# Kernel optimization log

Measured on AMD Instinct MI355X. Metric: run time of the kernel, lower is better.

## Reference

```python
import jax, jax.numpy as jnp
import numpy as np

D_MODEL = 1024
D_STATE = 16
D_CONV = 4
EXPAND = 2
HEADDIM = 64
NGROUPS = 1
D_INNER = EXPAND * D_MODEL            # 2048
NHEADS = D_INNER // HEADDIM           # 32
CONV_DIM = D_INNER + 2 * NGROUPS * D_STATE   # 2080
D_IN_PROJ = 2 * D_INNER + 2 * NGROUPS * D_STATE + NHEADS  # 4160
EPS = 1e-5
BATCH, SEQLEN = 4, 2048


def setup_inputs() -> dict:
    key = jax.random.key(0)
    ks = jax.random.split(key, 8)
    x = jax.random.normal(ks[0], (BATCH, SEQLEN, D_MODEL), jnp.float32)
    W_in = jax.random.normal(ks[1], (D_MODEL, D_IN_PROJ), jnp.float32) * 0.02
    conv_w = jax.random.normal(ks[2], (CONV_DIM, D_CONV), jnp.float32) * 0.2
    conv_b = jnp.zeros((CONV_DIM,), jnp.float32)
    # dt_bias = inverse softplus of dt drawn in [1e-3, 1e-1] (mamba_ssm init)
    dt = jax.random.uniform(ks[3], (NHEADS,), jnp.float32, 0.001, 0.1)
    dt_bias = jnp.log(jnp.expm1(dt))
    A_log = jnp.log(jax.random.uniform(ks[4], (NHEADS,), jnp.float32, 1.0, 16.0))
    D_param = jnp.ones((NHEADS,), jnp.float32)
    norm_w = jnp.ones((D_INNER,), jnp.float32)
    W_out = jax.random.normal(ks[5], (D_INNER, D_MODEL), jnp.float32) * 0.02
    layer_scale = jnp.full((D_MODEL,), 1e-4, jnp.float32)
    return dict(x=x, W_in=W_in, conv_w=conv_w, conv_b=conv_b, dt_bias=dt_bias,
                A_log=A_log, D_param=D_param, norm_w=norm_w, W_out=W_out,
                layer_scale=layer_scale)


def _silu(v):
    return v * jax.nn.sigmoid(v)


def _mamba2(x, W_in, conv_w, conv_b, dt_bias, A_log, D_param, norm_w, W_out):
    b, l, _ = x.shape
    zxbcdt = x @ W_in                                  # (b, l, d_in_proj)
    z = zxbcdt[..., :D_INNER]                          # gate
    xBC = zxbcdt[..., D_INNER:D_INNER + CONV_DIM]
    dt = jax.nn.softplus(zxbcdt[..., D_INNER + CONV_DIM:] + dt_bias)  # (b, l, h)
    # causal depthwise conv1d (kernel D_CONV) + SiLU
    xp = jnp.pad(xBC, ((0, 0), (D_CONV - 1, 0), (0, 0)))
    conv = sum(xp[:, k:k + l, :] * conv_w[:, k] for k in range(D_CONV)) + conv_b
    xBC = _silu(conv)
    xs = xBC[..., :D_INNER].reshape(b, l, NHEADS, HEADDIM)  # (b, l, h, p)
    Bm = xBC[..., D_INNER:D_INNER + D_STATE]                # (b, l, n), ngroups=1
    Cm = xBC[..., D_INNER + D_STATE:]                       # (b, l, n)
    A = -jnp.exp(A_log)                                     # (h,)
    dA = jnp.exp(dt * A)                                    # (b, l, h)
    dtx = dt[..., None] * xs                                # (b, l, h, p)

    def step(h, inp):
        dA_t, dtx_t, B_t, C_t = inp
        # h: (b, h, p, n)
        h = h * dA_t[..., None, None] + dtx_t[..., None] * B_t[:, None, None, :]
        y = jnp.einsum('bhpn,bn->bhp', h, C_t)
        return h, y

    h0 = jnp.zeros((b, NHEADS, HEADDIM, D_STATE), x.dtype)
    _, ys = jax.lax.scan(step, h0, (dA.transpose(1, 0, 2), dtx.transpose(1, 0, 2, 3),
                                    Bm.transpose(1, 0, 2), Cm.transpose(1, 0, 2)))
    y = ys.transpose(1, 0, 2, 3) + D_param[None, None, :, None] * xs  # (b, l, h, p)
    y = y.reshape(b, l, D_INNER)
    # gated RMSNorm (norm_before_gate=False): gate first, then rmsnorm
    y = y * _silu(z)
    y = y * jax.lax.rsqrt(jnp.mean(y * y, axis=-1, keepdims=True) + EPS) * norm_w
    return y @ W_out


def reference(x, W_in, conv_w, conv_b, dt_bias, A_log, D_param, norm_w, W_out, layer_scale):
    # dropout is identity (eval / p=0)
    return x + _mamba2(x, W_in, conv_w, conv_b, dt_bias, A_log, D_param, norm_w, W_out) * layer_scale
```

## Files before the change

### kernel.cpp

```cpp
#include <hip/hip_runtime.h>
#include <hip/hip_bf16.h>

#define D_MODEL   1024
#define D_STATE   16
#define D_CONV    4
#define HEADDIM   64
#define NHEADS    32
#define D_INNER   2048
#define CONV_DIM  2080
#define D_IN_PROJ 4160
#define NPAD      4224
#define BATCH     4
#define SEQLEN    2048
#define MROWS     (BATCH*SEQLEN)
#define QCHUNK    64
#define NCHUNK    (SEQLEN/QCHUNK)
#define DT_COL    (2*D_INNER + 2*D_STATE)

#define WSCALE    16.f
#define YSCALE    64.f

__device__ __forceinline__ unsigned short f2b(float f) {
    union { float f; unsigned int u; } v; v.f = f;
    unsigned int r = (v.u + 0x7FFFu + ((v.u >> 16) & 1u)) >> 16;
    return (unsigned short)r;
}
__device__ __forceinline__ float b2f(unsigned short h) {
    union { unsigned int u; float f; } v; v.u = ((unsigned int)h) << 16;
    return v.f;
}
__device__ __forceinline__ unsigned char f2fp8(float f) {
    return (unsigned char)(__builtin_amdgcn_cvt_pk_fp8_f32(f, 0.f, 0, false) & 0xFF);
}

typedef __attribute__((ext_vector_type(8))) short bf16x8;
typedef __attribute__((ext_vector_type(4))) float f32x4;
typedef __attribute__((ext_vector_type(4))) int   i32x4;
typedef __attribute__((ext_vector_type(8))) int   i32x8;

__device__ __forceinline__ i32x8 cat8(i32x4 a, i32x4 b) {
    i32x8 r;
    r[0] = a[0]; r[1] = a[1]; r[2] = a[2]; r[3] = a[3];
    r[4] = b[0]; r[5] = b[1]; r[6] = b[2]; r[7] = b[3];
    return r;
}

__device__ __forceinline__ void async_copy16b(const unsigned char* g, unsigned char* l) {
    __builtin_amdgcn_global_load_lds(
        (const __attribute__((address_space(1))) void*)g,
        (__attribute__((address_space(3))) void*)l, 16, 0, 0);
}

__global__ void cast_f32_fp8(const float* __restrict__ in, unsigned char* __restrict__ out, int n) {
    int i = (blockIdx.x * blockDim.x + threadIdx.x) * 4;
    if (i >= n) return;
    float4 v = *(const float4*)&in[i];
    int p = __builtin_amdgcn_cvt_pk_fp8_f32(v.x, v.y, 0, false);
    p = __builtin_amdgcn_cvt_pk_fp8_f32(v.z, v.w, p, true);
    *(unsigned int*)&out[i] = (unsigned int)p;
}

__global__ void transpose_both(const float* __restrict__ W_in, unsigned char* __restrict__ winT,
                               const float* __restrict__ W_out, unsigned char* __restrict__ woutT,
                               const float* __restrict__ norm_w) {
    __shared__ float tile[64][65];
    int bid = blockIdx.x;
    const float* W; unsigned char* WT; const float* kscale;
    int K, N, bx, by;
    if (bid < 1056) { W = W_in;  WT = winT;  kscale = nullptr; K = 1024; N = 4160; bx = bid % 66; by = bid / 66; }
    else { bid -= 1056; W = W_out; WT = woutT; kscale = norm_w; K = 2048; N = 1024; bx = bid % 16; by = bid / 16; }
    int n0 = bx * 64, k0 = by * 64;
    int tx = threadIdx.x & 63, ty = threadIdx.x >> 6;
    #pragma unroll
    for (int i = 0; i < 16; i++) {
        int r = ty * 16 + i;
        int n = n0 + tx;
        float v = (n < N) ? W[(size_t)(k0 + r) * N + n] : 0.f;
        tile[r][tx] = v;
    }
    __syncthreads();
    float ks = WSCALE * (kscale ? kscale[k0 + tx] : 1.f);
    #pragma unroll
    for (int i = 0; i < 16; i++) {
        int r = ty * 16 + i;
        WT[(size_t)(n0 + r) * K + k0 + tx] = f2fp8(tile[tx][r] * ks);
    }
}

template <int EPI>
__global__ __launch_bounds__(256)
void gemm_fp8(const unsigned char* __restrict__ A, const unsigned char* __restrict__ B,
              int K, int N, unsigned short* __restrict__ Cb,
              float* __restrict__ Cf, const float* __restrict__ xres,
              const float* __restrict__ ls, const float* __restrict__ rs) {
    __shared__ unsigned char lds_a[128 * 128];
    __shared__ unsigned char lds_b[128 * 128];
    const int tid  = threadIdx.x;
    const int wave = tid >> 6;
    const int lane = tid & 63;
    const int bid = blockIdx.x;
    const int xcd = bid & 7, g = bid >> 3;
    const int bm = xcd * 8 + (g & 7);
    const int bn = g >> 3;
    const int wm = wave >> 1, wn = wave & 1;

    f32x4 acc[4][4];
    #pragma unroll
    for (int i = 0; i < 4; i++)
        #pragma unroll
        for (int j = 0; j < 4; j++) acc[i][j] = (f32x4){0.f, 0.f, 0.f, 0.f};

    const int srow = lane >> 3;
    const int sseg = (lane & 7) ^ srow;
    const unsigned char* gA0 = A + (size_t)(bm * 128 + wave * 8 + srow) * K + sseg * 16;
    const unsigned char* gB0 = B + (size_t)(bn * 128 + wave * 8 + srow) * K + sseg * 16;
    const int ldsbase = wave * 8 * 128;

    const int lm = lane & 15, q = lane >> 4;

    for (int k0 = 0; k0 < K; k0 += 128) {
        #pragma unroll
        for (int j = 0; j < 4; j++) {
            async_copy16b(gA0 + k0 + (size_t)(j * 32) * K, &lds_a[ldsbase + j * 32 * 128]);
            async_copy16b(gB0 + k0 + (size_t)(j * 32) * K, &lds_b[ldsbase + j * 32 * 128]);
        }
        __syncthreads();

        i32x8 af[4], bfr[4];
        #pragma unroll
        for (int i = 0; i < 4; i++) {
            int r = wm * 64 + i * 16 + lm;
            int s0 = ((2 * q) ^ (r & 7)) * 16, s1 = ((2 * q + 1) ^ (r & 7)) * 16;
            af[i] = cat8(*(const i32x4*)&lds_a[r * 128 + s0],
                         *(const i32x4*)&lds_a[r * 128 + s1]);
        }
        #pragma unroll
        for (int j = 0; j < 4; j++) {
            int r = wn * 64 + j * 16 + lm;
            int s0 = ((2 * q) ^ (r & 7)) * 16, s1 = ((2 * q + 1) ^ (r & 7)) * 16;
            bfr[j] = cat8(*(const i32x4*)&lds_b[r * 128 + s0],
                          *(const i32x4*)&lds_b[r * 128 + s1]);
        }
        #pragma unroll
        for (int i = 0; i < 4; i++)
            #pragma unroll
            for (int j = 0; j < 4; j++)
                acc[i][j] = __builtin_amdgcn_mfma_scale_f32_16x16x128_f8f6f4(
                    af[i], bfr[j], acc[i][j], 0, 0,
                    0, 0x7F7F7F7F, 0, 0x7F7F7F7F);
        __syncthreads();
    }

    const int row0 = bm * 128 + wm * 64;
    const int col0 = bn * 128 + wn * 64;
    const int lq = (lane >> 4) * 4;
    #pragma unroll
    for (int i = 0; i < 4; i++) {
        #pragma unroll
        for (int j = 0; j < 4; j++) {
            #pragma unroll
            for (int r = 0; r < 4; r++) {
                int gr = row0 + i * 16 + lq + r;
                int gc = col0 + j * 16 + lm;
                float v = acc[i][j][r];
                if (EPI == 0) {
                    Cb[(size_t)gr * N + gc] = f2b(v * (1.f / WSCALE));
                } else {
                    size_t idx = (size_t)gr * 1024 + gc;
                    Cf[idx] = xres[idx] + v * ls[gc] * rs[gr] * (1.f / (WSCALE * YSCALE));
                }
            }
        }
    }
}

__global__ __launch_bounds__(256)
void ssd_hcomp(const unsigned short* __restrict__ zx, const float* __restrict__ dt_bias,
               const float* __restrict__ conv_w, const float* __restrict__ conv_b,
               const float* __restrict__ A_log,
               float* __restrict__ hbuf, float* __restrict__ pbuf,
               unsigned short* __restrict__ xTg, unsigned short* __restrict__ bcg,
               float* __restrict__ scA) {
    __shared__ unsigned short sXraw[67 * 64];
    __shared__ unsigned short sBCraw[67 * 32];
    __shared__ unsigned short sXT[64 * 72];
    __shared__ unsigned short sBC[64 * 32];
    __shared__ unsigned short sBwT[16 * 72];
    __shared__ float sdt[64], scd[64];

    const int blk = blockIdx.x;
    const int c  = blk & 31;
    const int h  = (blk >> 5) & 31;
    const int b  = blk >> 10;
    const int bh = blk >> 5;
    const int row0 = b * SEQLEN + c * QCHUNK;
    const int batch0 = b * SEQLEN;

    const int t    = threadIdx.x;
    const int w    = t >> 6;
    const int lane = t & 63;
    const int lm   = lane & 15;
    const int lq8  = (lane >> 4) * 8;
    const int lq4  = (lane >> 4) * 4;
    const float Ah = -__expf(A_log[h]);

    for (int i = t; i < 536; i += 256) {
        int r = i >> 3, seg = i & 7;
        int gr = row0 - 3 + r;
        int4 v = (gr >= batch0) ? *(const int4*)&zx[(size_t)gr * NPAD + D_INNER + h * 64 + seg * 8]
                                : (int4){0, 0, 0, 0};
        *(int4*)&sXraw[r * 64 + seg * 8] = v;
    }
    for (int i = t; i < 268; i += 256) {
        int r = i >> 2, seg = i & 3;
        int gr = row0 - 3 + r;
        int4 v = (gr >= batch0) ? *(const int4*)&zx[(size_t)gr * NPAD + 2 * D_INNER + seg * 8]
                                : (int4){0, 0, 0, 0};
        *(int4*)&sBCraw[r * 32 + seg * 8] = v;
    }
    if (t < 64) {
        float raw = b2f(zx[(size_t)(row0 + t) * NPAD + DT_COL + h]) + dt_bias[h];
        float dtv = (raw > 20.f) ? raw : log1pf(__expf(raw));
        float v = dtv;
        #pragma unroll
        for (int o = 1; o < 64; o <<= 1) {
            float u = __shfl_up(v, o, 64);
            if (t >= o) v += u;
        }
        sdt[t] = dtv;
        scd[t] = v;
        float sc = __expf(Ah * v);
        float* scrow = &scA[(size_t)(bh * NCHUNK + c) * 192];
        scrow[t] = dtv; scrow[64 + t] = v; scrow[128 + t] = sc;
        if (t == 63) pbuf[bh * NCHUNK + c] = sc;
    }
    __syncthreads();

    {
        const int p = t & 63, sblk = (t >> 6) * 16;
        const int ch = h * 64 + p;
        const float4 cw = *(const float4*)&conv_w[ch * 4];
        const float cb = conv_b[ch];
        float x0 = b2f(sXraw[(sblk + 0) * 64 + p]);
        float x1 = b2f(sXraw[(sblk + 1) * 64 + p]);
        float x2 = b2f(sXraw[(sblk + 2) * 64 + p]);
        #pragma unroll
        for (int i = 0; i < 16; i++) {
            float x3 = b2f(sXraw[(sblk + i + 3) * 64 + p]);
            float acc = cb + cw.x * x0 + cw.y * x1 + cw.z * x2 + cw.w * x3;
            float sv = acc / (1.f + __expf(-acc));
            sXT[p * 72 + sblk + i] = f2b(sv);
            x0 = x1; x1 = x2; x2 = x3;
        }
    }
    {
        const int ch32 = t & 31, s0 = (t >> 5) * 8;
        const int ch = D_INNER + ch32;
        const float4 cw = *(const float4*)&conv_w[ch * 4];
        const float cb = conv_b[ch];
        const float cdl = scd[63];
        float x0 = b2f(sBCraw[(s0 + 0) * 32 + ch32]);
        float x1 = b2f(sBCraw[(s0 + 1) * 32 + ch32]);
        float x2 = b2f(sBCraw[(s0 + 2) * 32 + ch32]);
        #pragma unroll
        for (int i = 0; i < 8; i++) {
            int s = s0 + i;
            float x3 = b2f(sBCraw[(s + 3) * 32 + ch32]);
            float acc = cb + cw.x * x0 + cw.y * x1 + cw.z * x2 + cw.w * x3;
            float sv = acc / (1.f + __expf(-acc));
            sBC[s * 32 + ch32] = f2b(sv);
            if (ch32 < 16) {
                float wgt = sdt[s] * __expf(Ah * (cdl - scd[s]));
                sBwT[ch32 * 72 + s] = f2b(sv * wgt);
            }
            x0 = x1; x1 = x2; x2 = x3;
        }
    }
    __syncthreads();

    f32x4 hacc = (f32x4){0.f, 0.f, 0.f, 0.f};
    #pragma unroll
    for (int ks = 0; ks < 2; ks++) {
        bf16x8 af = *(const bf16x8*)&sBwT[lm * 72 + ks * 32 + lq8];
        bf16x8 bf_ = *(const bf16x8*)&sXT[(w * 16 + lm) * 72 + ks * 32 + lq8];
        hacc = __builtin_amdgcn_mfma_f32_16x16x32_bf16(af, bf_, hacc, 0, 0, 0);
    }
    #pragma unroll
    for (int r = 0; r < 4; r++)
        hbuf[(size_t)(bh * NCHUNK + c) * 1024 + (lq4 + r) * 64 + (w * 16 + lm)] = hacc[r];

    #pragma unroll
    for (int it = 0; it < 2; it++) {
        int idx = t + it * 256;
        int p = idx >> 3, seg = idx & 7;
        *(int4*)&xTg[(size_t)(bh * 64 + p) * SEQLEN + c * 64 + seg * 8] =
            *(const int4*)&sXT[p * 72 + seg * 8];
    }
    if (h == 0) {
        int s = t >> 2, seg = t & 3;
        *(int4*)&bcg[(size_t)(b * SEQLEN + c * 64 + s) * 32 + seg * 8] =
            *(const int4*)&sBC[s * 32 + seg * 8];
    }
}

__global__ __launch_bounds__(1024)
void ssd_state_scan(float* __restrict__ hbuf, const float* __restrict__ pbuf) {
    int bh = blockIdx.x;
    int t = threadIdx.x;
    __shared__ float sP[NCHUNK];
    if (t < NCHUNK) sP[t] = pbuf[bh * NCHUNK + t];
    __syncthreads();
    size_t base = (size_t)bh * NCHUNK * 1024 + t;
    float v[NCHUNK];
    #pragma unroll
    for (int c = 0; c < NCHUNK; c++) v[c] = hbuf[base + (size_t)c * 1024];
    float carry = 0.f;
    #pragma unroll
    for (int c = 0; c < NCHUNK; c++) {
        float tmp = v[c];
        v[c] = carry;
        carry = tmp + sP[c] * carry;
    }
    #pragma unroll
    for (int c = 0; c < NCHUNK; c++) hbuf[base + (size_t)c * 1024] = v[c];
}

__global__ __launch_bounds__(256)
void ssd_yfused(const unsigned short* __restrict__ zx,
                const unsigned short* __restrict__ xTg, const unsigned short* __restrict__ bcg,
                const float* __restrict__ scA,
                const float* __restrict__ A_log, const float* __restrict__ D_param,
                const float* __restrict__ hbuf,
                unsigned char* __restrict__ y, float* __restrict__ ssq) {
    __shared__ unsigned short sXT[64 * 72];
    __shared__ unsigned short sM[64 * 72];
    __shared__ unsigned short sB[64 * 32];
    __shared__ unsigned short sC[64 * 32];
    __shared__ unsigned short sZ[64 * 64];
    __shared__ unsigned short sHT[64 * 40];
    __shared__ float sdt[64], scd[64], sSc[64];

    const int blk = blockIdx.x;
    const int c  = blk & 31;
    const int h  = (blk >> 5) & 31;
    const int b  = blk >> 10;
    const int bh = blk >> 5;
    const int row0 = b * SEQLEN + c * QCHUNK;

    const int t    = threadIdx.x;
    const int w    = t >> 6;
    const int lane = t & 63;
    const int lm   = lane & 15;
    const int lq8  = (lane >> 4) * 8;
    const int lq4  = (lane >> 4) * 4;
    const float Ah = -__expf(A_log[h]);

    #pragma unroll
    for (int it = 0; it < 2; it++) {
        int idx = t + it * 256;
        int p = idx >> 3, seg = idx & 7;
        *(int4*)&sXT[p * 72 + seg * 8] =
            *(const int4*)&xTg[(size_t)(bh * 64 + p) * SEQLEN + c * 64 + seg * 8];
    }
    #pragma unroll
    for (int it = 0; it < 2; it++) {
        int idx = t + it * 256;
        int s = idx >> 3, seg = idx & 7;
        *(int4*)&sZ[s * 64 + seg * 8] =
            *(const int4*)&zx[(size_t)(row0 + s) * NPAD + h * 64 + seg * 8];
    }
    {
        int s = t >> 2, seg = t & 3;
        int4 v = *(const int4*)&bcg[(size_t)(b * SEQLEN + c * 64 + s) * 32 + seg * 8];
        if (seg < 2) *(int4*)&sB[s * 32 + seg * 8] = v;
        else         *(int4*)&sC[s * 32 + (seg - 2) * 8] = v;
    }
    {
        size_t hb = (size_t)(bh * NCHUNK + c) * 1024 + (size_t)t * 4;
        float4 hv = *(const float4*)&hbuf[hb];
        int n = t >> 4;
        int p0 = (t * 4) & 63;
        sHT[(p0 + 0) * 40 + n] = f2b(hv.x);
        sHT[(p0 + 1) * 40 + n] = f2b(hv.y);
        sHT[(p0 + 2) * 40 + n] = f2b(hv.z);
        sHT[(p0 + 3) * 40 + n] = f2b(hv.w);
    }
    if (t < 64) {
        *(int4*)&sB[t * 32 + 16] = (int4){0, 0, 0, 0};
        *(int4*)&sB[t * 32 + 24] = (int4){0, 0, 0, 0};
        *(int4*)&sC[t * 32 + 16] = (int4){0, 0, 0, 0};
        *(int4*)&sC[t * 32 + 24] = (int4){0, 0, 0, 0};
        *(int4*)&sHT[t * 40 + 16] = (int4){0, 0, 0, 0};
        *(int4*)&sHT[t * 40 + 24] = (int4){0, 0, 0, 0};
    }
    if (t < 192) {
        float v = scA[(size_t)(bh * NCHUNK + c) * 192 + t];
        if (t < 64) sdt[t] = v;
        else if (t < 128) scd[t - 64] = v;
        else sSc[t - 128] = v;
    }
    __syncthreads();

    f32x4 sacc[4];
    {
        bf16x8 cfrag = *(const bf16x8*)&sC[(w * 16 + lm) * 32 + lq8];
        #pragma unroll
        for (int sb = 0; sb < 4; sb++) {
            if (sb <= w) {
                bf16x8 bfrag = *(const bf16x8*)&sB[(sb * 16 + lm) * 32 + lq8];
                sacc[sb] = __builtin_amdgcn_mfma_f32_16x16x32_bf16(
                    cfrag, bfrag, (f32x4){0.f, 0.f, 0.f, 0.f}, 0, 0, 0);
            }
        }
    }
    const float Dh = D_param[h];
    #pragma unroll
    for (int sb = 0; sb < 4; sb++) {
        int sp = sb * 16 + lm;
        if (sb > w) {
            #pragma unroll
            for (int r = 0; r < 4; r++) sM[(w * 16 + lq4 + r) * 72 + sp] = 0;
        } else {
            float dts = sdt[sp], cds = scd[sp];
            #pragma unroll
            for (int r = 0; r < 4; r++) {
                int tp = w * 16 + lq4 + r;
                float m = 0.f;
                if (sb < w || sp <= tp) {
                    m = sacc[sb][r] * dts * __expf(Ah * (scd[tp] - cds));
                    if (sp == tp) m += Dh;
                }
                sM[tp * 72 + sp] = f2b(m);
            }
        }
    }

    f32x4 yacc[4];
    #pragma unroll
    for (int pb = 0; pb < 4; pb++) yacc[pb] = (f32x4){0.f, 0.f, 0.f, 0.f};
    #pragma unroll
    for (int ks = 0; ks < 2; ks++) {
        if (ks == 1 && w < 2) continue;
        bf16x8 af = *(const bf16x8*)&sM[(w * 16 + lm) * 72 + ks * 32 + lq8];
        #pragma unroll
        for (int pb = 0; pb < 4; pb++) {
            bf16x8 bf_ = *(const bf16x8*)&sXT[(pb * 16 + lm) * 72 + ks * 32 + lq8];
            yacc[pb] = __builtin_amdgcn_mfma_f32_16x16x32_bf16(af, bf_, yacc[pb], 0, 0, 0);
        }
    }
    f32x4 acc2[4];
    {
        bf16x8 cf2 = *(const bf16x8*)&sC[(w * 16 + lm) * 32 + lq8];
        #pragma unroll
        for (int pb = 0; pb < 4; pb++) {
            bf16x8 hf = *(const bf16x8*)&sHT[(pb * 16 + lm) * 40 + lq8];
            acc2[pb] = __builtin_amdgcn_mfma_f32_16x16x32_bf16(
                cf2, hf, (f32x4){0.f, 0.f, 0.f, 0.f}, 0, 0, 0);
        }
    }

    #pragma unroll
    for (int r = 0; r < 4; r++) {
        const int tp = w * 16 + lq4 + r;
        const size_t yrow = (size_t)(row0 + tp) * D_INNER + h * 64;
        float ssr = 0.f;
        #pragma unroll
        for (int pb = 0; pb < 4; pb++) {
            int pp = pb * 16 + lm;
            float val = yacc[pb][r] + sSc[tp] * acc2[pb][r];
            float zv = b2f(sZ[tp * 64 + pp]);
            float yg = val * (zv / (1.f + __expf(-zv)));
            ssr += yg * yg;
            y[yrow + pp] = f2fp8(yg * YSCALE);
        }
        ssr += __shfl_xor(ssr, 1, 16);
        ssr += __shfl_xor(ssr, 2, 16);
        ssr += __shfl_xor(ssr, 4, 16);
        ssr += __shfl_xor(ssr, 8, 16);
        if (lm == 0)
            ssq[(size_t)(row0 + tp) * NHEADS + h] = ssr;
    }
}

__global__ __launch_bounds__(256)
void rowscale_kernel(const float* __restrict__ ssq, float* __restrict__ rs) {
    int row = blockIdx.x * 256 + threadIdx.x;
    const float4* p = (const float4*)&ssq[(size_t)row * NHEADS];
    float s = 0.f;
    #pragma unroll
    for (int i = 0; i < 8; i++) {
        float4 v = p[i];
        s += v.x + v.y + v.z + v.w;
    }
    rs[row] = rsqrtf(s * (1.f / D_INNER) + 1e-5f);
}

extern "C" void kernel_launch(void* const* d_in, const int* in_sizes, int n_in,
                              void* d_out, int out_size, void* d_ws, size_t ws_size,
                              hipStream_t stream) {
    const float* x        = (const float*)d_in[0];
    const float* W_in     = (const float*)d_in[1];
    const float* conv_w   = (const float*)d_in[2];
    const float* conv_b   = (const float*)d_in[3];
    const float* dt_bias  = (const float*)d_in[4];
    const float* A_log    = (const float*)d_in[5];
    const float* D_param  = (const float*)d_in[6];
    const float* norm_w   = (const float*)d_in[7];
    const float* W_out    = (const float*)d_in[8];
    const float* ls       = (const float*)d_in[9];
    float* out = (float*)d_out;

    char* ws = (char*)d_ws;
    size_t off = 0;
    unsigned char*  x_f8  = (unsigned char*)(ws + off);  off += (size_t)MROWS * D_MODEL;
    unsigned char*  winT  = (unsigned char*)(ws + off);  off += (size_t)NPAD * D_MODEL;
    unsigned char*  woutT = (unsigned char*)(ws + off);  off += (size_t)D_MODEL * D_INNER;
    unsigned short* zx    = (unsigned short*)(ws + off); off += (size_t)MROWS * NPAD * 2;
    float*          pbuf  = (float*)(ws + off);          off += (size_t)BATCH * NHEADS * NCHUNK * 4;
    unsigned char*  yb    = (unsigned char*)(ws + off);  off += (size_t)MROWS * D_INNER;
    float*          ssq   = (float*)(ws + off);          off += (size_t)MROWS * NHEADS * 4;
    float*          rsb   = (float*)(ws + off);          off += (size_t)MROWS * 4;
    float*          hbuf  = (float*)(ws + off);          off += (size_t)BATCH * NHEADS * NCHUNK * 1024 * 4;
    unsigned short* xTg   = (unsigned short*)(ws + off); off += (size_t)MROWS * D_INNER * 2;
    unsigned short* bcg   = (unsigned short*)(ws + off); off += (size_t)MROWS * 32 * 2;
    float*          scA   = (float*)(ws + off);          off += (size_t)BATCH * NHEADS * NCHUNK * 192 * 4;

    cast_f32_fp8<<<(MROWS * D_MODEL) / 1024, 256, 0, stream>>>(x, x_f8, MROWS * D_MODEL);
    transpose_both<<<1568, 256, 0, stream>>>(W_in, winT, W_out, woutT, norm_w);
    gemm_fp8<0><<<(NPAD / 128) * 64, 256, 0, stream>>>(
        x_f8, winT, D_MODEL, NPAD, zx, nullptr, nullptr, nullptr, nullptr);
    ssd_hcomp<<<BATCH * NHEADS * NCHUNK, 256, 0, stream>>>(
        zx, dt_bias, conv_w, conv_b, A_log, hbuf, pbuf, xTg, bcg, scA);
    ssd_state_scan<<<BATCH * NHEADS, 1024, 0, stream>>>(hbuf, pbuf);
    ssd_yfused<<<BATCH * NHEADS * NCHUNK, 256, 0, stream>>>(
        zx, xTg, bcg, scA, A_log, D_param, hbuf, yb, ssq);
    rowscale_kernel<<<MROWS / 256, 256, 0, stream>>>(ssq, rsb);
    gemm_fp8<1><<<(D_MODEL / 128) * 64, 256, 0, stream>>>(
        yb, woutT, D_INNER, D_MODEL, nullptr, out, x, ls, rsb);
}
```

Baseline: 262.0 us.

## Rewrite FP8 GEMM with double-buffered LDS, 256x128 tiles and interleaved MFMA/loads

```diff
diff --git a/kernel.cpp b/kernel.cpp
--- a/kernel.cpp
+++ b/kernel.cpp
@@ -51,6 +51,11 @@
         (__attribute__((address_space(3))) void*)l, 16, 0, 0);
 }
 
+__device__ __forceinline__ void sbar() {
+    __builtin_amdgcn_s_barrier();
+    asm volatile("" ::: "memory");
+}
+
 __global__ void cast_f32_fp8(const float* __restrict__ in, unsigned char* __restrict__ out, int n) {
     int i = (blockIdx.x * blockDim.x + threadIdx.x) * 4;
     if (i >= n) return;
@@ -88,21 +93,26 @@
 }
 
 template <int EPI>
-__global__ __launch_bounds__(256)
-void gemm_fp8(const unsigned char* __restrict__ A, const unsigned char* __restrict__ B,
-              int K, int N, unsigned short* __restrict__ Cb,
-              float* __restrict__ Cf, const float* __restrict__ xres,
-              const float* __restrict__ ls, const float* __restrict__ rs) {
-    __shared__ unsigned char lds_a[128 * 128];
-    __shared__ unsigned char lds_b[128 * 128];
+__global__ __launch_bounds__(512, 2)
+void gemm8p(const unsigned char* __restrict__ A, const unsigned char* __restrict__ B,
+            int K, int N, unsigned short* __restrict__ Cb,
+            float* __restrict__ Cf, const float* __restrict__ xres,
+            const float* __restrict__ ls, const float* __restrict__ rs) {
+    __shared__ unsigned char la[2][256 * 128];
+    __shared__ unsigned char lb[2][128 * 128];
     const int tid  = threadIdx.x;
     const int wave = tid >> 6;
     const int lane = tid & 63;
-    const int bid = blockIdx.x;
-    const int xcd = bid & 7, g = bid >> 3;
-    const int bm = xcd * 8 + (g & 7);
-    const int bn = g >> 3;
-    const int wm = wave >> 1, wn = wave & 1;
+
+    const int cpx = gridDim.x >> 3;
+    const int wg  = (blockIdx.x & 7) * cpx + (blockIdx.x >> 3);
+    const int bm  = wg & 31;
+    const int bn  = wg >> 5;
+
+    const int wm = wave >> 1;
+    const int wn = wave & 1;
+    const int lm = lane & 15, q = lane >> 4;
+    const int lq4 = q * 4;
 
     f32x4 acc[4][4];
     #pragma unroll
@@ -112,59 +122,82 @@
 
     const int srow = lane >> 3;
     const int sseg = (lane & 7) ^ srow;
-    const unsigned char* gA0 = A + (size_t)(bm * 128 + wave * 8 + srow) * K + sseg * 16;
-    const unsigned char* gB0 = B + (size_t)(bn * 128 + wave * 8 + srow) * K + sseg * 16;
-    const int ldsbase = wave * 8 * 128;
-
-    const int lm = lane & 15, q = lane >> 4;
-
-    for (int k0 = 0; k0 < K; k0 += 128) {
-        #pragma unroll
-        for (int j = 0; j < 4; j++) {
-            async_copy16b(gA0 + k0 + (size_t)(j * 32) * K, &lds_a[ldsbase + j * 32 * 128]);
-            async_copy16b(gB0 + k0 + (size_t)(j * 32) * K, &lds_b[ldsbase + j * 32 * 128]);
-        }
-        __syncthreads();
-
-        i32x8 af[4], bfr[4];
-        #pragma unroll
-        for (int i = 0; i < 4; i++) {
-            int r = wm * 64 + i * 16 + lm;
-            int s0 = ((2 * q) ^ (r & 7)) * 16, s1 = ((2 * q + 1) ^ (r & 7)) * 16;
-            af[i] = cat8(*(const i32x4*)&lds_a[r * 128 + s0],
-                         *(const i32x4*)&lds_a[r * 128 + s1]);
-        }
-        #pragma unroll
-        for (int j = 0; j < 4; j++) {
-            int r = wn * 64 + j * 16 + lm;
-            int s0 = ((2 * q) ^ (r & 7)) * 16, s1 = ((2 * q + 1) ^ (r & 7)) * 16;
-            bfr[j] = cat8(*(const i32x4*)&lds_b[r * 128 + s0],
-                          *(const i32x4*)&lds_b[r * 128 + s1]);
-        }
-        #pragma unroll
-        for (int i = 0; i < 4; i++)
-            #pragma unroll
-            for (int j = 0; j < 4; j++)
-                acc[i][j] = __builtin_amdgcn_mfma_scale_f32_16x16x128_f8f6f4(
-                    af[i], bfr[j], acc[i][j], 0, 0,
-                    0, 0x7F7F7F7F, 0, 0x7F7F7F7F);
-        __syncthreads();
-    }
-
-    const int row0 = bm * 128 + wm * 64;
+    const unsigned char* gA = A + (size_t)(bm * 256 + wave * 8 + srow) * K + sseg * 16;
+    const unsigned char* gB = B + (size_t)(bn * 128 + wave * 8 + srow) * K + sseg * 16;
+    const int ldsb = wave * 8 * 128;
+
+#define SA(kt, d, g) async_copy16b(gA + (kt) * 128 + (size_t)((g) * 64) * K, &la[d][((g) * 64) * 128 + ldsb])
+#define SB(kt, d, g) async_copy16b(gB + (kt) * 128 + (size_t)((g) * 64) * K, &lb[d][((g) * 64) * 128 + ldsb])
+#define RDA(dst, i) do { const int r_ = wm * 64 + (i) * 16 + lm; \
+    const int s0_ = ((2 * q) ^ (r_ & 7)) * 16, s1_ = ((2 * q + 1) ^ (r_ & 7)) * 16; \
+    dst = cat8(*(const i32x4*)&la[cur][r_ * 128 + s0_], *(const i32x4*)&la[cur][r_ * 128 + s1_]); } while (0)
+#define RDB(dst, j) do { const int r_ = wn * 64 + (j) * 16 + lm; \
+    const int s0_ = ((2 * q) ^ (r_ & 7)) * 16, s1_ = ((2 * q + 1) ^ (r_ & 7)) * 16; \
+    dst = cat8(*(const i32x4*)&lb[cur][r_ * 128 + s0_], *(const i32x4*)&lb[cur][r_ * 128 + s1_]); } while (0)
+#define MM(i, j) acc[i][j] = __builtin_amdgcn_mfma_scale_f32_16x16x128_f8f6f4( \
+    af[i], bf[j], acc[i][j], 0, 0, 0, 0x7F7F7F7F, 0, 0x7F7F7F7F)
+
+    const int NT = K >> 7;
+    SA(0, 0, 0); SA(0, 0, 1); SA(0, 0, 2); SA(0, 0, 3);
+    SB(0, 0, 0); SB(0, 0, 1);
+
+    i32x8 af[4], bf[4];
+    for (int t = 0; t < NT; ++t) {
+        const int cur = t & 1, nxt = cur ^ 1;
+        sbar();
+        if (t + 1 < NT) {
+            SA(t + 1, nxt, 0);
+            asm volatile("s_waitcnt vmcnt(1)" ::: "memory");
+        } else {
+            asm volatile("s_waitcnt vmcnt(0)" ::: "memory");
+        }
+        sbar();
+
+        RDA(af[0], 0); RDA(af[1], 1); RDB(bf[0], 0); RDB(bf[1], 1);
+        if (t + 1 < NT) { SA(t + 1, nxt, 1); SB(t + 1, nxt, 0); }
+        sbar();
+        __builtin_amdgcn_s_setprio(1);
+        MM(0, 0); MM(0, 1); MM(1, 0); MM(1, 1);
+        __builtin_amdgcn_s_setprio(0);
+        sbar();
+        RDA(af[2], 2); RDA(af[3], 3);
+        if (t + 1 < NT) { SA(t + 1, nxt, 2); SB(t + 1, nxt, 1); }
+        sbar();
+        __builtin_amdgcn_s_setprio(1);
+        MM(2, 0); MM(2, 1); MM(3, 0); MM(3, 1);
+        __builtin_amdgcn_s_setprio(0);
+        sbar();
+        RDB(bf[2], 2); RDB(bf[3], 3);
+        if (t + 1 < NT) { SA(t + 1, nxt, 3); }
+        sbar();
+        __builtin_amdgcn_s_setprio(1);
+        MM(2, 2); MM(2, 3); MM(3, 2); MM(3, 3);
+        __builtin_amdgcn_s_setprio(0);
+        sbar();
+        __builtin_amdgcn_s_setprio(1);
+        MM(0, 2); MM(0, 3); MM(1, 2); MM(1, 3);
+        __builtin_amdgcn_s_setprio(0);
+    }
+#undef SA
+#undef SB
+#undef RDA
+#undef RDB
+#undef MM
+
+    const int row0 = bm * 256 + wm * 64;
     const int col0 = bn * 128 + wn * 64;
-    const int lq = (lane >> 4) * 4;
     #pragma unroll
     for (int i = 0; i < 4; i++) {
         #pragma unroll
         for (int j = 0; j < 4; j++) {
             #pragma unroll
             for (int r = 0; r < 4; r++) {
-                int gr = row0 + i * 16 + lq + r;
+                int gr = row0 + i * 16 + lq4 + r;
                 int gc = col0 + j * 16 + lm;
                 float v = acc[i][j][r];
                 if (EPI == 0) {
-                    Cb[(size_t)gr * N + gc] = f2b(v * (1.f / WSCALE));
+                    if (gc < D_IN_PROJ)
+                        Cb[(size_t)gr * N + gc] = f2b(v * (1.f / WSCALE));
                 } else {
                     size_t idx = (size_t)gr * 1024 + gc;
                     Cf[idx] = xres[idx] + v * ls[gc] * rs[gr] * (1.f / (WSCALE * YSCALE));
@@ -527,7 +560,7 @@
 
     cast_f32_fp8<<<(MROWS * D_MODEL) / 1024, 256, 0, stream>>>(x, x_f8, MROWS * D_MODEL);
     transpose_both<<<1568, 256, 0, stream>>>(W_in, winT, W_out, woutT, norm_w);
-    gemm_fp8<0><<<(NPAD / 128) * 64, 256, 0, stream>>>(
+    gemm8p<0><<<1056, 512, 0, stream>>>(
         x_f8, winT, D_MODEL, NPAD, zx, nullptr, nullptr, nullptr, nullptr);
     ssd_hcomp<<<BATCH * NHEADS * NCHUNK, 256, 0, stream>>>(
         zx, dt_bias, conv_w, conv_b, A_log, hbuf, pbuf, xTg, bcg, scA);
@@ -535,6 +568,6 @@
     ssd_yfused<<<BATCH * NHEADS * NCHUNK, 256, 0, stream>>>(
         zx, xTg, bcg, scA, A_log, D_param, hbuf, yb, ssq);
     rowscale_kernel<<<MROWS / 256, 256, 0, stream>>>(ssq, rsb);
-    gemm_fp8<1><<<(D_MODEL / 128) * 64, 256, 0, stream>>>(
-        yb, woutT, D_INNER, D_MODEL, nullptr, out, x, ls, rsb);
-}
+    gemm8p<1><<<256, 512, 0, stream>>>(
+        yb, woutT, 2 * D_MODEL, D_MODEL, nullptr, out, x, ls, rsb);
+}
```

Measured after the change: 318.8 us. 1.22x slower.
